# Kernel tuning notes

Measured on AMD Instinct MI355X. Metric: run time of the kernel, lower is better.

Reference implementation:

```python
import jax, jax.numpy as jnp
import numpy as np

VOCAB, D, SLOTS, K = 50257, 512, 16, 3
B, T_FULL = 64, 2049
EPS_LN = 1e-5


def setup_inputs() -> dict:
    key = jax.random.key(0)
    ks = jax.random.split(key, 12)
    u = jax.random.uniform(ks[0], (B, T_FULL - 1), jnp.float32)
    gumbel = -jnp.log(-jnp.log(u + 1e-8) + 1e-8)
    s = 0.02
    return {
        "seq": jax.random.randint(ks[1], (B, T_FULL), 0, VOCAB),
        "temperature": jnp.ones((), jnp.float32),
        "gumbel": gumbel,
        "embed": jax.random.normal(ks[2], (VOCAB, D), jnp.float32) * s,
        "W1": jax.random.normal(ks[3], (D, 2 * D), jnp.float32) * s,
        "b1": jnp.zeros((2 * D,), jnp.float32),
        "W2": jax.random.normal(ks[4], (2 * D, D), jnp.float32) * s,
        "b2": jnp.zeros((D,), jnp.float32),
        "gamma": jnp.ones((D,), jnp.float32),
        "beta": jnp.zeros((D,), jnp.float32),
        "Wg": jax.random.normal(ks[5], (D,), jnp.float32) * s,
        "bg": jnp.zeros((), jnp.float32),
        "Wr": jax.random.normal(ks[6], (D, D), jnp.float32) * s,
        "br": jnp.zeros((D,), jnp.float32),
        "Wo": jax.random.normal(ks[7], (D, VOCAB), jnp.float32) * s,
        "bo": jnp.zeros((VOCAB,), jnp.float32),
    }


def reference(seq, temperature, gumbel, embed, W1, b1, W2, b2, gamma, beta, Wg, bg, Wr, br, Wo, bo):
    # Encoder: embed -> FFN residual -> LayerNorm
    h = embed[seq]                                        # [B, T+1, D]
    ff = jnp.maximum(h @ W1 + b1, 0.0) @ W2 + b2
    x = h + ff
    mu = jnp.mean(x, -1, keepdims=True)
    var = jnp.mean((x - mu) ** 2, -1, keepdims=True)
    hiddens = (x - mu) * jax.lax.rsqrt(var + EPS_LN) * gamma + beta

    context = hiddens[:, :-1, :]                          # [B, T, D]
    gate = context @ Wg + bg                              # [B, T]

    # gumbel top-k with straight-through mask (forward value = hard mask)
    perturbed = (gate + gumbel) / temperature
    _, idx = jax.lax.top_k(perturbed, K)                  # [B, K]
    mask = jnp.zeros_like(gate).at[jnp.arange(B)[:, None], idx].set(1.0)
    soft = jax.nn.softmax(perturbed, axis=-1)
    sel = mask + soft - jax.lax.stop_gradient(soft)

    # gather selected hidden states, scatter_add into memory slots
    gw = jnp.take_along_axis(sel, idx, axis=1)            # [B, K]
    gh = jnp.take_along_axis(context, idx[..., None], axis=1)  # [B, K, D]
    weighted = gh * gw[..., None]
    slot_idx = jnp.arange(K) % SLOTS
    mem = jnp.zeros((B, SLOTS, D), hiddens.dtype).at[:, slot_idx, :].add(weighted)

    # attention read with last-position query
    q = hiddens[:, -1, :] @ Wr + br                       # [B, D]
    scores = jnp.einsum('bsd,bd->bs', mem, q)
    attn = jax.nn.softmax(scores, axis=-1)
    ctx = jnp.einsum('bs,bsd->bd', attn, mem)
    return ctx @ Wo + bo                                  # [B, vocab]
```

## Files before the change

kernel.cpp:

```cpp
#include <hip/hip_runtime.h>
#include <math.h>

#define TFULL 2049
#define TCTX  2048
#define Vm    50257

#define KBS 1032

typedef __attribute__((ext_vector_type(8))) short bf16x8;
typedef __attribute__((ext_vector_type(4))) short s16x4;
typedef __attribute__((ext_vector_type(4))) float f32x4;

__device__ __forceinline__ float wred64(float v){
  #pragma unroll
  for (int m = 1; m < 64; m <<= 1) v += __shfl_xor(v, m, 64);
  return v;
}
__device__ __forceinline__ short bf16_rn(float x){
  union { float f; unsigned u; } c; c.f = x;
  unsigned r = c.u + 0x7fff + ((c.u >> 16) & 1);
  return (short)(r >> 16);
}
__device__ __forceinline__ float bf16_f(short s){
  union { float f; unsigned u; } c; c.u = ((unsigned)(unsigned short)s) << 16;
  return c.f;
}

#define FMA4(ACC_, S_, W_)                         \
  (ACC_).x = fmaf((S_), (W_).x, (ACC_).x);         \
  (ACC_).y = fmaf((S_), (W_).y, (ACC_).y);         \
  (ACC_).z = fmaf((S_), (W_).z, (ACC_).z);         \
  (ACC_).w = fmaf((S_), (W_).w, (ACC_).w);

__global__ void k0_setup(const float* __restrict__ gamma, const float* __restrict__ beta,
                         const float* __restrict__ Wg, float* __restrict__ scal){
  const int t = threadIdx.x;
  float wg = Wg[t];
  float g  = gamma[t]*wg, bw = beta[t]*wg;
  scal[2 + t] = g;
  g = wred64(g); bw = wred64(bw);
  __shared__ float ra[8], rb[8];
  if ((t & 63) == 0){ ra[t>>6] = g; rb[t>>6] = bw; }
  __syncthreads();
  if (t == 0){
    float G = 0.f, Bw = 0.f;
    #pragma unroll
    for (int i = 0; i < 8; ++i){ G += ra[i]; Bw += rb[i]; }
    scal[0] = G; scal[1] = Bw;
  }
}

__global__ __launch_bounds__(256) void kpack(const float* __restrict__ W, int N, int KB,
                                             short* __restrict__ hi, short* __restrict__ lo){
  int i = blockIdx.x*256 + threadIdx.x;
  if (i >= KB*N*4) return;
  int kq = i & 3;
  int n  = (i >> 2) % N;
  int kb = i / (N*4);
  const float* src = W + (kb*32 + kq*8)*N + n;
  bf16x8 h8, l8;
  #pragma unroll
  for (int j = 0; j < 8; ++j){
    float w = src[j*N];
    short h = bf16_rn(w);
    h8[j] = h;
    l8[j] = bf16_rn(w - bf16_f(h));
  }
  *(bf16x8*)(hi + i*8) = h8;
  *(bf16x8*)(lo + i*8) = l8;
}

__global__ __launch_bounds__(512, 4) void k1_main(
    const int*   __restrict__ seq,   const float* __restrict__ temp,
    const float* __restrict__ gumbel,const float* __restrict__ embed,
    const short* __restrict__ W1h,   const short* __restrict__ W1l,
    const float* __restrict__ b1,
    const short* __restrict__ W2h,   const short* __restrict__ W2l,
    const float* __restrict__ b2,
    const float* __restrict__ gamma, const float* __restrict__ beta,
    const float* __restrict__ bg,
    const float* __restrict__ scal,
    float* __restrict__ pert, float* __restrict__ qh)
{
  __shared__ __align__(16) short Ah[8*KBS];
  __shared__ __align__(16) short Al[8*KBS];
  __shared__ __align__(16) short Rbuf[2*8*KBS];
  __shared__ float Xq[512];
  __shared__ int   srow[32];
  __shared__ float redS1[256], redS2[256], redSG[256];
  __shared__ float redMu[32], redRs[32];

  short* Rh = Rbuf;
  short* Rl = Rbuf + 8*KBS;

  const int t    = threadIdx.x;
  const int tile = blockIdx.x;
  const int lane = t & 63;
  const int wv   = t >> 6;
  const int mrow = lane & 15;
  const int kq   = lane >> 4;
  const int crow0 = kq*4;

  const int lane_sw = kq*128 + ((mrow & 12) | ((mrow ^ kq) & 3))*8;

  if (t < 32) srow[t] = seq[tile*32 + t];
  __syncthreads();

  const f32x4* __restrict__ embv = (const f32x4*)embed;

  auto stageA = [&](int hh){
    #pragma unroll
    for (int k = 0; k < 4; ++k){
      int idx = k*512 + t;
      int tok = idx >> 6, c4 = idx & 63;
      f32x4 v = embv[srow[tok]*128 + hh*64 + c4];
      int kbr = c4 >> 3, kqw = (c4 >> 1) & 3, j0 = (c4 & 1)*4;
      int tokL = tok & 15, mt = tok >> 4;
      int base = kbr*KBS + mt*512 + kqw*128
               + ((tokL & 12) | ((tokL ^ kqw) & 3))*8 + j0;
      short h0 = bf16_rn(v[0]), h1 = bf16_rn(v[1]), h2 = bf16_rn(v[2]), h3 = bf16_rn(v[3]);
      *(s16x4*)(Ah + base) = (s16x4){h0, h1, h2, h3};
      *(s16x4*)(Al + base) = (s16x4){ bf16_rn(v[0] - bf16_f(h0)),
                                      bf16_rn(v[1] - bf16_f(h1)),
                                      bf16_rn(v[2] - bf16_f(h2)),
                                      bf16_rn(v[3] - bf16_f(h3)) };
    }
  };

  f32x4 ff[4][2];
  #pragma unroll
  for (int i = 0; i < 4; ++i)
    #pragma unroll
    for (int j = 0; j < 2; ++j) ff[i][j] = (f32x4){0.f,0.f,0.f,0.f};

  int boff2[4];
  #pragma unroll
  for (int nt = 0; nt < 4; ++nt)
    boff2[nt] = (wv*64 + nt*16 + mrow)*32 + kq*8;

  #pragma unroll 1
  for (int ch = 0; ch < 4; ++ch){
    f32x4 acc[2][2];
    #pragma unroll
    for (int i = 0; i < 2; ++i)
      #pragma unroll
      for (int j = 0; j < 2; ++j) acc[i][j] = (f32x4){0.f,0.f,0.f,0.f};

    int boff1[2];
    #pragma unroll
    for (int nt = 0; nt < 2; ++nt)
      boff1[nt] = (ch*256 + wv*32 + nt*16 + mrow)*32 + kq*8;

    auto g1 = [&](int hh){
      const short* whB = W1h + hh*262144;
      const short* wlB = W1l + hh*262144;
      #pragma unroll
      for (int kbr = 0; kbr < 8; ++kbr){
        bf16x8 ah0 = *(const bf16x8*)(Ah + kbr*KBS + lane_sw);
        bf16x8 al0 = *(const bf16x8*)(Al + kbr*KBS + lane_sw);
        bf16x8 ah1 = *(const bf16x8*)(Ah + kbr*KBS + 512 + lane_sw);
        bf16x8 al1 = *(const bf16x8*)(Al + kbr*KBS + 512 + lane_sw);
        #pragma unroll
        for (int nt = 0; nt < 2; ++nt){
          bf16x8 bh = *(const bf16x8*)(whB + kbr*32768 + boff1[nt]);
          bf16x8 bl = *(const bf16x8*)(wlB + kbr*32768 + boff1[nt]);
          acc[nt][0] = __builtin_amdgcn_mfma_f32_16x16x32_bf16(ah0, bh, acc[nt][0], 0,0,0);
          acc[nt][0] = __builtin_amdgcn_mfma_f32_16x16x32_bf16(al0, bh, acc[nt][0], 0,0,0);
          acc[nt][0] = __builtin_amdgcn_mfma_f32_16x16x32_bf16(ah0, bl, acc[nt][0], 0,0,0);
          acc[nt][1] = __builtin_amdgcn_mfma_f32_16x16x32_bf16(ah1, bh, acc[nt][1], 0,0,0);
          acc[nt][1] = __builtin_amdgcn_mfma_f32_16x16x32_bf16(al1, bh, acc[nt][1], 0,0,0);
          acc[nt][1] = __builtin_amdgcn_mfma_f32_16x16x32_bf16(ah1, bl, acc[nt][1], 0,0,0);
        }
      }
    };

    stageA(0);
    __syncthreads();
    g1(0);
    __syncthreads();
    stageA(1);
    __syncthreads();
    g1(1);
    __syncthreads();

    #pragma unroll
    for (int nt = 0; nt < 2; ++nt){
      int jcol = wv*32 + nt*16 + mrow;
      float bb = b1[ch*256 + jcol];
      int kb2 = jcol >> 5, kq2 = (jcol >> 3) & 3, j2 = jcol & 7;
      int rbase = kb2*KBS + kq2*128 + j2;
      #pragma unroll
      for (int mt = 0; mt < 2; ++mt){
        #pragma unroll
        for (int r = 0; r < 4; ++r){
          int tokL = crow0 + r;
          int off = rbase + mt*512 + ((tokL & 12) | ((tokL ^ kq2) & 3))*8;
          float a = fmaxf(acc[nt][mt][r] + bb, 0.f);
          short h = bf16_rn(a);
          Rh[off] = h;
          Rl[off] = bf16_rn(a - bf16_f(h));
        }
      }
    }
    __syncthreads();

    {
      const short* w2hB = W2h + ch*131072;
      const short* w2lB = W2l + ch*131072;
      #pragma unroll
      for (int kb = 0; kb < 8; ++kb){
        bf16x8 rh0 = *(const bf16x8*)(Rh + kb*KBS + lane_sw);
        bf16x8 rl0 = *(const bf16x8*)(Rl + kb*KBS + lane_sw);
        bf16x8 rh1 = *(const bf16x8*)(Rh + kb*KBS + 512 + lane_sw);
        bf16x8 rl1 = *(const bf16x8*)(Rl + kb*KBS + 512 + lane_sw);
        #pragma unroll
        for (int nt = 0; nt < 4; ++nt){
          bf16x8 bh = *(const bf16x8*)(w2hB + kb*16384 + boff2[nt]);
          bf16x8 bl = *(const bf16x8*)(w2lB + kb*16384 + boff2[nt]);
          ff[nt][0] = __builtin_amdgcn_mfma_f32_16x16x32_bf16(rh0, bh, ff[nt][0], 0,0,0);
          ff[nt][0] = __builtin_amdgcn_mfma_f32_16x16x32_bf16(rl0, bh, ff[nt][0], 0,0,0);
          ff[nt][0] = __builtin_amdgcn_mfma_f32_16x16x32_bf16(rh0, bl, ff[nt][0], 0,0,0);
          ff[nt][1] = __builtin_amdgcn_mfma_f32_16x16x32_bf16(rh1, bh, ff[nt][1], 0,0,0);
          ff[nt][1] = __builtin_amdgcn_mfma_f32_16x16x32_bf16(rl1, bh, ff[nt][1], 0,0,0);
          ff[nt][1] = __builtin_amdgcn_mfma_f32_16x16x32_bf16(rh1, bl, ff[nt][1], 0,0,0);
        }
      }
    }
  }

  __syncthreads();
  float* hbuf = (float*)Rbuf;
  #pragma unroll
  for (int k = 0; k < 4; ++k){
    int idx = k*512 + t;
    int tok = idx >> 6, c4 = idx & 63;
    f32x4 v = embv[srow[tok]*128 + c4];
    f32x4 hv;
    #pragma unroll
    for (int j = 0; j < 4; ++j){
      short hi = bf16_rn(v[j]);
      hv[j] = bf16_f(hi) + bf16_f(bf16_rn(v[j] - bf16_f(hi)));
    }
    *(f32x4*)(hbuf + tok*256 + c4*4) = hv;
  }
  __syncthreads();

  const float G1 = scal[0], BW = scal[1];
  const float* gWg = scal + 2;
  const float bgv  = bg[0];
  const float invT = 1.0f / temp[0];
  int rem  = (tile*32) % 2049;
  int qtok = 2048 - rem;

  float ps1[2][4], ps2[2][4], psg[2][4];
  #pragma unroll
  for (int mt = 0; mt < 2; ++mt)
    #pragma unroll
    for (int r = 0; r < 4; ++r){ ps1[mt][r]=0.f; ps2[mt][r]=0.f; psg[mt][r]=0.f; }

  #pragma unroll
  for (int nt = 0; nt < 4; ++nt){
    int d = wv*64 + nt*16 + mrow;
    float b2v = b2[d];
    float gw  = gWg[d];
    if (wv >= 4){
      int dl = d - 256;
      int kbr = dl >> 5, kq2 = (dl >> 3) & 3, jj = dl & 7;
      int abase = kbr*KBS + kq2*128 + jj;
      #pragma unroll
      for (int mt = 0; mt < 2; ++mt){
        #pragma unroll
        for (int r = 0; r < 4; ++r){
          int tokL = crow0 + r;
          int tok  = mt*16 + tokL;
          int off  = abase + mt*512 + ((tokL & 12) | ((tokL ^ kq2) & 3))*8;
          float h = bf16_f(Ah[off]) + bf16_f(Al[off]);
          float x = h + ff[nt][mt][r] + b2v;
          ps1[mt][r] += x;
          ps2[mt][r] = fmaf(x, x, ps2[mt][r]);
          psg[mt][r] = fmaf(x, gw, psg[mt][r]);
          if (tok == qtok) Xq[d] = x;
        }
      }
    } else {
      #pragma unroll
      for (int mt = 0; mt < 2; ++mt){
        #pragma unroll
        for (int r = 0; r < 4; ++r){
          int tok = mt*16 + crow0 + r;
          float h = hbuf[tok*256 + d];
          float x = h + ff[nt][mt][r] + b2v;
          ps1[mt][r] += x;
          ps2[mt][r] = fmaf(x, x, ps2[mt][r]);
          psg[mt][r] = fmaf(x, gw, psg[mt][r]);
          if (tok == qtok) Xq[d] = x;
        }
      }
    }
  }
  #pragma unroll
  for (int mt = 0; mt < 2; ++mt){
    #pragma unroll
    for (int r = 0; r < 4; ++r){
      float a = ps1[mt][r], b = ps2[mt][r], c = psg[mt][r];
      #pragma unroll
      for (int m = 1; m < 16; m <<= 1){
        a += __shfl_xor(a, m, 64);
        b += __shfl_xor(b, m, 64);
        c += __shfl_xor(c, m, 64);
      }
      if (mrow == 0){
        int tok = mt*16 + crow0 + r;
        redS1[tok*8 + wv] = a;
        redS2[tok*8 + wv] = b;
        redSG[tok*8 + wv] = c;
      }
    }
  }
  __syncthreads();

  if (t < 32){
    float S1 = 0.f, S2 = 0.f, SG = 0.f;
    #pragma unroll
    for (int w = 0; w < 8; ++w){
      S1 += redS1[t*8 + w];
      S2 += redS2[t*8 + w];
      SG += redSG[t*8 + w];
    }
    float mu  = S1 * (1.f/512.f);
    float var = S2 * (1.f/512.f) - mu*mu;
    float rs  = rsqrtf(var + 1e-5f);
    redMu[t] = mu; redRs[t] = rs;
    int id  = tile*32 + t;
    int b   = id / 2049;
    int pos = id - b*2049;
    if (pos < TCTX){
      float gate = rs*(SG - mu*G1) + BW + bgv;
      float pv = (gate + __builtin_nontemporal_load(gumbel + b*TCTX + pos)) * invT;
      __builtin_nontemporal_store(pv, pert + b*TCTX + pos);
    }
  }
  __syncthreads();

  if (qtok < 32 && t < 256){
    int id = tile*32 + qtok;
    int b  = id / 2049;
    float mu = redMu[qtok], rs = redRs[qtok];
    int d = t*2;
    qh[b*512 + d]     = (Xq[d]  -mu)*rs*gamma[d]   + beta[d];
    qh[b*512 + d + 1] = (Xq[d+1]-mu)*rs*gamma[d+1] + beta[d+1];
  }
}

__global__ __launch_bounds__(256) void k2_topk(const float* __restrict__ pert,
                                               int* __restrict__ idxw){
  __shared__ float v[2048];
  __shared__ float wvv[256];
  __shared__ int   wii[256];
  const int b = blockIdx.x, t = threadIdx.x;
  for (int i = t; i < 2048; i += 256) v[i] = pert[b*TCTX + i];
  __syncthreads();
  for (int r = 0; r < 3; ++r){
    float best = -INFINITY; int bi = 1<<30;
    for (int i = t; i < 2048; i += 256){
      float x = v[i];
      if (x > best || (x == best && i < bi)){ best = x; bi = i; }
    }
    wvv[t] = best; wii[t] = bi;
    __syncthreads();
    for (int s = 128; s > 0; s >>= 1){
      if (t < s){
        float ov = wvv[t+s]; int oi = wii[t+s];
        if (ov > wvv[t] || (ov == wvv[t] && oi < wii[t])){ wvv[t] = ov; wii[t] = oi; }
      }
      __syncthreads();
    }
    if (t == 0){ idxw[b*3 + r] = wii[0]; v[wii[0]] = -INFINITY; }
    __syncthreads();
  }
}

__global__ __launch_bounds__(256) void k3_rows(const int* __restrict__ seq,
    const float* __restrict__ embed, const float* __restrict__ W1, const float* __restrict__ b1,
    const float* __restrict__ W2,    const float* __restrict__ b2,
    const float* __restrict__ gamma, const float* __restrict__ beta,
    const int* __restrict__ idxw, float* __restrict__ memr)
{
  __shared__ float hs[3*512];
  __shared__ float rbuf[3*1024];
  __shared__ float red1[12], red2[12];
  const int t  = threadIdx.x;
  const int b  = blockIdx.x;
  const int wv = t >> 6;
  #pragma unroll
  for (int kk = 0; kk < 3; ++kk){
    int pos = idxw[b*3 + kk];
    int row = seq[b*TFULL + pos];
    ((float2*)(hs + kk*512))[t] = ((const float2*)(embed + row*512))[t];
  }
  __syncthreads();
  const float4* W1v = (const float4*)W1;
  float4 a0 = make_float4(0,0,0,0), a1 = a0, a2 = a0;
  #pragma unroll 2
  for (int d = 0; d < 512; ++d){
    float4 wq = W1v[d*256 + t];
    float h0 = hs[d], h1 = hs[512+d], h2 = hs[1024+d];
    FMA4(a0, h0, wq); FMA4(a1, h1, wq); FMA4(a2, h2, wq);
  }
  float4 bq = ((const float4*)b1)[t];
  float4 r0, r1, r2;
  r0.x = fmaxf(a0.x+bq.x,0.f); r0.y = fmaxf(a0.y+bq.y,0.f);
  r0.z = fmaxf(a0.z+bq.z,0.f); r0.w = fmaxf(a0.w+bq.w,0.f);
  r1.x = fmaxf(a1.x+bq.x,0.f); r1.y = fmaxf(a1.y+bq.y,0.f);
  r1.z = fmaxf(a1.z+bq.z,0.f); r1.w = fmaxf(a1.w+bq.w,0.f);
  r2.x = fmaxf(a2.x+bq.x,0.f); r2.y = fmaxf(a2.y+bq.y,0.f);
  r2.z = fmaxf(a2.z+bq.z,0.f); r2.w = fmaxf(a2.w+bq.w,0.f);
  ((float4*)rbuf)[t]          = r0;
  ((float4*)(rbuf+1024))[t]   = r1;
  ((float4*)(rbuf+2048))[t]   = r2;
  __syncthreads();
  const float2* W2v2 = (const float2*)W2;
  float f0x=0.f,f0y=0.f,f1x=0.f,f1y=0.f,f2x=0.f,f2y=0.f;
  #pragma unroll 2
  for (int j = 0; j < 1024; ++j){
    float2 wq = W2v2[j*256 + t];
    float q0 = rbuf[j], q1 = rbuf[1024+j], q2 = rbuf[2048+j];
    f0x = fmaf(q0, wq.x, f0x); f0y = fmaf(q0, wq.y, f0y);
    f1x = fmaf(q1, wq.x, f1x); f1y = fmaf(q1, wq.y, f1y);
    f2x = fmaf(q2, wq.x, f2x); f2y = fmaf(q2, wq.y, f2y);
  }
  float2 b2q = ((const float2*)b2)[t];
  const int dd = t*2;
  float2 hx0 = ((float2*)hs)[t];
  float2 hx1 = ((float2*)(hs+512))[t];
  float2 hx2 = ((float2*)(hs+1024))[t];
  float x00 = hx0.x + f0x + b2q.x, x01 = hx0.y + f0y + b2q.y;
  float x10 = hx1.x + f1x + b2q.x, x11 = hx1.y + f1y + b2q.y;
  float x20 = hx2.x + f2x + b2q.x, x21 = hx2.y + f2y + b2q.y;
  float s10 = wred64(x00 + x01), s20 = wred64(x00*x00 + x01*x01);
  float s11 = wred64(x10 + x11), s21 = wred64(x10*x10 + x11*x11);
  float s12 = wred64(x20 + x21), s22 = wred64(x20*x20 + x21*x21);
  if ((t & 63) == 0){
    red1[0*4+wv] = s10; red2[0*4+wv] = s20;
    red1[1*4+wv] = s11; red2[1*4+wv] = s21;
    red1[2*4+wv] = s12; red2[2*4+wv] = s22;
  }
  __syncthreads();
  float gx = gamma[dd], gy = gamma[dd+1], bx = beta[dd], by = beta[dd+1];
  #pragma unroll
  for (int kk = 0; kk < 3; ++kk){
    float S1 = red1[kk*4+0]+red1[kk*4+1]+red1[kk*4+2]+red1[kk*4+3];
    float S2 = red2[kk*4+0]+red2[kk*4+1]+red2[kk*4+2]+red2[kk*4+3];
    float mu  = S1*(1.f/512.f);
    float var = S2*(1.f/512.f) - mu*mu;
    float rs  = rsqrtf(var + 1e-5f);
    float x0 = (kk==0) ? x00 : (kk==1) ? x10 : x20;
    float x1 = (kk==0) ? x01 : (kk==1) ? x11 : x21;
    memr[(b*3+kk)*512 + dd]     = (x0-mu)*rs*gx + bx;
    memr[(b*3+kk)*512 + dd + 1] = (x1-mu)*rs*gy + by;
  }
}

__global__ __launch_bounds__(256) void k4_attn(const float* __restrict__ qh,
    const float* __restrict__ Wr, const float* __restrict__ br,
    const float* __restrict__ memr, float* __restrict__ ctxT)
{
  __shared__ float hq[512];
  __shared__ float red[12];
  const int t = threadIdx.x, b = blockIdx.x;
  ((float2*)hq)[t] = ((const float2*)(qh + b*512))[t];
  __syncthreads();
  const float2* Wrv = (const float2*)Wr;
  float qx = 0.f, qy = 0.f;
  #pragma unroll 4
  for (int d = 0; d < 512; ++d){
    float hb = hq[d];
    float2 wq = Wrv[d*256 + t];
    qx = fmaf(hb, wq.x, qx); qy = fmaf(hb, wq.y, qy);
  }
  float2 brq = ((const float2*)br)[t];
  qx += brq.x; qy += brq.y;
  const int dd = t*2;
  const float* m0 = memr + (b*3+0)*512;
  const float* m1 = memr + (b*3+1)*512;
  const float* m2 = memr + (b*3+2)*512;
  float p0 = wred64(qx*m0[dd] + qy*m0[dd+1]);
  float p1 = wred64(qx*m1[dd] + qy*m1[dd+1]);
  float p2 = wred64(qx*m2[dd] + qy*m2[dd+1]);
  if ((t & 63) == 0){ int w = t>>6; red[w*3+0]=p0; red[w*3+1]=p1; red[w*3+2]=p2; }
  __syncthreads();
  float s0 = red[0]+red[3]+red[6]+red[9];
  float s1 = red[1]+red[4]+red[7]+red[10];
  float s2 = red[2]+red[5]+red[8]+red[11];
  float m  = fmaxf(fmaxf(s0, s1), fmaxf(s2, 0.f));
  float e0 = expf(s0-m), e1 = expf(s1-m), e2 = expf(s2-m);
  float den = e0 + e1 + e2 + 13.f*expf(-m);
  float a0 = e0/den, a1 = e1/den, a2 = e2/den;
  float c0 = a0*m0[dd]   + a1*m1[dd]   + a2*m2[dd];
  float c1 = a0*m0[dd+1] + a1*m1[dd+1] + a2*m2[dd+1];
  ctxT[dd*64 + b]     = c0;
  ctxT[(dd+1)*64 + b] = c1;
}

__global__ __launch_bounds__(256) void k5_out(const float* __restrict__ ctxT,
    const float* __restrict__ Wo, const float* __restrict__ bo,
    float* __restrict__ out)
{
  const int v  = blockIdx.x*256 + threadIdx.x;
  const int vc = v < Vm ? v : Vm-1;
  float acc[64];
  #pragma unroll
  for (int b = 0; b < 64; ++b) acc[b] = 0.f;
  for (int d = 0; d < 512; ++d){
    float w = Wo[d*Vm + vc];
    const float* c = ctxT + d*64;
    #pragma unroll
    for (int b = 0; b < 64; ++b) acc[b] = fmaf(c[b], w, acc[b]);
  }
  if (v < Vm){
    float bb = bo[v];
    #pragma unroll
    for (int b = 0; b < 64; ++b) out[b*Vm + v] = acc[b] + bb;
  }
}

extern "C" void kernel_launch(void* const* d_in, const int* in_sizes, int n_in,
                              void* d_out, int out_size, void* d_ws, size_t ws_size,
                              hipStream_t stream){
  (void)in_sizes; (void)n_in; (void)out_size; (void)ws_size;
  const int*   seq   = (const int*)d_in[0];
  const float* temp  = (const float*)d_in[1];
  const float* gum   = (const float*)d_in[2];
  const float* embed = (const float*)d_in[3];
  const float* W1    = (const float*)d_in[4];
  const float* b1    = (const float*)d_in[5];
  const float* W2    = (const float*)d_in[6];
  const float* b2    = (const float*)d_in[7];
  const float* gamma = (const float*)d_in[8];
  const float* beta  = (const float*)d_in[9];
  const float* Wg    = (const float*)d_in[10];
  const float* bg    = (const float*)d_in[11];
  const float* Wr    = (const float*)d_in[12];
  const float* br    = (const float*)d_in[13];
  const float* Wo    = (const float*)d_in[14];
  const float* bo    = (const float*)d_in[15];
  float* out = (float*)d_out;

  float* wsf  = (float*)d_ws;
  float* pert = wsf;
  float* qh   = wsf + 131072;
  float* memr = wsf + 163840;
  float* ctxT = wsf + 262144;
  float* scal = wsf + 294912;
  int*   idxw = (int*)(wsf + 295936);
  short* W1h  = (short*)(wsf + 296192);
  short* W1l  = W1h + 512*1024;
  short* W2h  = W1l + 512*1024;
  short* W2l  = W2h + 1024*512;

  k0_setup<<<1, 512, 0, stream>>>(gamma, beta, Wg, scal);
  kpack<<<256, 256, 0, stream>>>(W1, 1024, 16, W1h, W1l);
  kpack<<<256, 256, 0, stream>>>(W2, 512, 32, W2h, W2l);
  k1_main<<<4098, 512, 0, stream>>>(seq, temp, gum, embed, W1h, W1l, b1,
                                    W2h, W2l, b2, gamma, beta, bg, scal, pert, qh);
  k2_topk<<<64, 256, 0, stream>>>(pert, idxw);
  k3_rows<<<64, 256, 0, stream>>>(seq, embed, W1, b1, W2, b2, gamma, beta, idxw, memr);
  k4_attn<<<64, 256, 0, stream>>>(qh, Wr, br, memr, ctxT);
  k5_out<<<197, 256, 0, stream>>>(ctxT, Wo, bo, out);
}
```

Baseline: 2.071 ms.

## Stage full embedding tile once in LDS and reuse across all chunks

```diff
diff --git a/kernel.cpp b/kernel.cpp
--- a/kernel.cpp
+++ b/kernel.cpp
@@ -70,7 +70,7 @@
   *(bf16x8*)(lo + i*8) = l8;
 }
 
-__global__ __launch_bounds__(512, 4) void k1_main(
+__global__ __launch_bounds__(512, 2) void k1_main(
     const int*   __restrict__ seq,   const float* __restrict__ temp,
     const float* __restrict__ gumbel,const float* __restrict__ embed,
     const short* __restrict__ W1h,   const short* __restrict__ W1l,
@@ -82,8 +82,8 @@
     const float* __restrict__ scal,
     float* __restrict__ pert, float* __restrict__ qh)
 {
-  __shared__ __align__(16) short Ah[8*KBS];
-  __shared__ __align__(16) short Al[8*KBS];
+  __shared__ __align__(16) short Ah[16*KBS];
+  __shared__ __align__(16) short Al[16*KBS];
   __shared__ __align__(16) short Rbuf[2*8*KBS];
   __shared__ float Xq[512];
   __shared__ int   srow[32];
@@ -108,24 +108,23 @@
 
   const f32x4* __restrict__ embv = (const f32x4*)embed;
 
-  auto stageA = [&](int hh){
-    #pragma unroll
-    for (int k = 0; k < 4; ++k){
-      int idx = k*512 + t;
-      int tok = idx >> 6, c4 = idx & 63;
-      f32x4 v = embv[srow[tok]*128 + hh*64 + c4];
-      int kbr = c4 >> 3, kqw = (c4 >> 1) & 3, j0 = (c4 & 1)*4;
-      int tokL = tok & 15, mt = tok >> 4;
-      int base = kbr*KBS + mt*512 + kqw*128
-               + ((tokL & 12) | ((tokL ^ kqw) & 3))*8 + j0;
-      short h0 = bf16_rn(v[0]), h1 = bf16_rn(v[1]), h2 = bf16_rn(v[2]), h3 = bf16_rn(v[3]);
-      *(s16x4*)(Ah + base) = (s16x4){h0, h1, h2, h3};
-      *(s16x4*)(Al + base) = (s16x4){ bf16_rn(v[0] - bf16_f(h0)),
-                                      bf16_rn(v[1] - bf16_f(h1)),
-                                      bf16_rn(v[2] - bf16_f(h2)),
-                                      bf16_rn(v[3] - bf16_f(h3)) };
-    }
-  };
+  #pragma unroll
+  for (int k = 0; k < 8; ++k){
+    int idx = k*512 + t;
+    int tok = idx >> 7, c4 = idx & 127;
+    f32x4 v = embv[srow[tok]*128 + c4];
+    int kbr = c4 >> 3, kqw = (c4 >> 1) & 3, j0 = (c4 & 1)*4;
+    int tokL = tok & 15, mt = tok >> 4;
+    int base = kbr*KBS + mt*512 + kqw*128
+             + ((tokL & 12) | ((tokL ^ kqw) & 3))*8 + j0;
+    short h0 = bf16_rn(v[0]), h1 = bf16_rn(v[1]), h2 = bf16_rn(v[2]), h3 = bf16_rn(v[3]);
+    *(s16x4*)(Ah + base) = (s16x4){h0, h1, h2, h3};
+    *(s16x4*)(Al + base) = (s16x4){ bf16_rn(v[0] - bf16_f(h0)),
+                                    bf16_rn(v[1] - bf16_f(h1)),
+                                    bf16_rn(v[2] - bf16_f(h2)),
+                                    bf16_rn(v[3] - bf16_f(h3)) };
+  }
+  __syncthreads();
 
   f32x4 ff[4][2];
   #pragma unroll
@@ -151,36 +150,25 @@
     for (int nt = 0; nt < 2; ++nt)
       boff1[nt] = (ch*256 + wv*32 + nt*16 + mrow)*32 + kq*8;
 
-    auto g1 = [&](int hh){
-      const short* whB = W1h + hh*262144;
-      const short* wlB = W1l + hh*262144;
+    #pragma unroll 4
+    for (int kbr = 0; kbr < 16; ++kbr){
+      bf16x8 ah0 = *(const bf16x8*)(Ah + kbr*KBS + lane_sw);
+      bf16x8 al0 = *(const bf16x8*)(Al + kbr*KBS + lane_sw);
+      bf16x8 ah1 = *(const bf16x8*)(Ah + kbr*KBS + 512 + lane_sw);
+      bf16x8 al1 = *(const bf16x8*)(Al + kbr*KBS + 512 + lane_sw);
       #pragma unroll
-      for (int kbr = 0; kbr < 8; ++kbr){
-        bf16x8 ah0 = *(const bf16x8*)(Ah + kbr*KBS + lane_sw);
-        bf16x8 al0 = *(const bf16x8*)(Al + kbr*KBS + lane_sw);
-        bf16x8 ah1 = *(const bf16x8*)(Ah + kbr*KBS + 512 + lane_sw);
-        bf16x8 al1 = *(const bf16x8*)(Al + kbr*KBS + 512 + lane_sw);
-        #pragma unroll
-        for (int nt = 0; nt < 2; ++nt){
-          bf16x8 bh = *(const bf16x8*)(whB + kbr*32768 + boff1[nt]);
-          bf16x8 bl = *(const bf16x8*)(wlB + kbr*32768 + boff1[nt]);
-          acc[nt][0] = __builtin_amdgcn_mfma_f32_16x16x32_bf16(ah0, bh, acc[nt][0], 0,0,0);
-          acc[nt][0] = __builtin_amdgcn_mfma_f32_16x16x32_bf16(al0, bh, acc[nt][0], 0,0,0);
-          acc[nt][0] = __builtin_amdgcn_mfma_f32_16x16x32_bf16(ah0, bl, acc[nt][0], 0,0,0);
-          acc[nt][1] = __builtin_amdgcn_mfma_f32_16x16x32_bf16(ah1, bh, acc[nt][1], 0,0,0);
-          acc[nt][1] = __builtin_amdgcn_mfma_f32_16x16x32_bf16(al1, bh, acc[nt][1], 0,0,0);
-          acc[nt][1] = __builtin_amdgcn_mfma_f32_16x16x32_bf16(ah1, bl, acc[nt][1], 0,0,0);
-        }
-      }
-    };
-
-    stageA(0);
-    __syncthreads();
-    g1(0);
-    __syncthreads();
-    stageA(1);
-    __syncthreads();
-    g1(1);
+      for (int nt = 0; nt < 2; ++nt){
+        bf16x8 bh = *(const bf16x8*)(W1h + kbr*32768 + boff1[nt]);
+        bf16x8 bl = *(const bf16x8*)(W1l + kbr*32768 + boff1[nt]);
+        acc[nt][0] = __builtin_amdgcn_mfma_f32_16x16x32_bf16(ah0, bh, acc[nt][0], 0,0,0);
+        acc[nt][0] = __builtin_amdgcn_mfma_f32_16x16x32_bf16(al0, bh, acc[nt][0], 0,0,0);
+        acc[nt][0] = __builtin_amdgcn_mfma_f32_16x16x32_bf16(ah0, bl, acc[nt][0], 0,0,0);
+        acc[nt][1] = __builtin_amdgcn_mfma_f32_16x16x32_bf16(ah1, bh, acc[nt][1], 0,0,0);
+        acc[nt][1] = __builtin_amdgcn_mfma_f32_16x16x32_bf16(al1, bh, acc[nt][1], 0,0,0);
+        acc[nt][1] = __builtin_amdgcn_mfma_f32_16x16x32_bf16(ah1, bl, acc[nt][1], 0,0,0);
+      }
+    }
+
     __syncthreads();
 
     #pragma unroll
@@ -207,7 +195,7 @@
     {
       const short* w2hB = W2h + ch*131072;
       const short* w2lB = W2l + ch*131072;
-      #pragma unroll
+      #pragma unroll 2
       for (int kb = 0; kb < 8; ++kb){
         bf16x8 rh0 = *(const bf16x8*)(Rh + kb*KBS + lane_sw);
         bf16x8 rl0 = *(const bf16x8*)(Rl + kb*KBS + lane_sw);
@@ -228,23 +216,6 @@
     }
   }
 
-  __syncthreads();
-  float* hbuf = (float*)Rbuf;
-  #pragma unroll
-  for (int k = 0; k < 4; ++k){
-    int idx = k*512 + t;
-    int tok = idx >> 6, c4 = idx & 63;
-    f32x4 v = embv[srow[tok]*128 + c4];
-    f32x4 hv;
-    #pragma unroll
-    for (int j = 0; j < 4; ++j){
-      short hi = bf16_rn(v[j]);
-      hv[j] = bf16_f(hi) + bf16_f(bf16_rn(v[j] - bf16_f(hi)));
-    }
-    *(f32x4*)(hbuf + tok*256 + c4*4) = hv;
-  }
-  __syncthreads();
-
   const float G1 = scal[0], BW = scal[1];
   const float* gWg = scal + 2;
   const float bgv  = bg[0];
@@ -263,38 +234,21 @@
     int d = wv*64 + nt*16 + mrow;
     float b2v = b2[d];
     float gw  = gWg[d];
-    if (wv >= 4){
-      int dl = d - 256;
-      int kbr = dl >> 5, kq2 = (dl >> 3) & 3, jj = dl & 7;
-      int abase = kbr*KBS + kq2*128 + jj;
+    int kb  = d >> 5, kq2 = (d >> 3) & 3, jj = d & 7;
+    int abase = kb*KBS + kq2*128 + jj;
+    #pragma unroll
+    for (int mt = 0; mt < 2; ++mt){
       #pragma unroll
-      for (int mt = 0; mt < 2; ++mt){
-        #pragma unroll
-        for (int r = 0; r < 4; ++r){
-          int tokL = crow0 + r;
-          int tok  = mt*16 + tokL;
-          int off  = abase + mt*512 + ((tokL & 12) | ((tokL ^ kq2) & 3))*8;
-          float h = bf16_f(Ah[off]) + bf16_f(Al[off]);
-          float x = h + ff[nt][mt][r] + b2v;
-          ps1[mt][r] += x;
-          ps2[mt][r] = fmaf(x, x, ps2[mt][r]);
-          psg[mt][r] = fmaf(x, gw, psg[mt][r]);
-          if (tok == qtok) Xq[d] = x;
-        }
-      }
-    } else {
-      #pragma unroll
-      for (int mt = 0; mt < 2; ++mt){
-        #pragma unroll
-        for (int r = 0; r < 4; ++r){
-          int tok = mt*16 + crow0 + r;
-          float h = hbuf[tok*256 + d];
-          float x = h + ff[nt][mt][r] + b2v;
-          ps1[mt][r] += x;
-          ps2[mt][r] = fmaf(x, x, ps2[mt][r]);
-          psg[mt][r] = fmaf(x, gw, psg[mt][r]);
-          if (tok == qtok) Xq[d] = x;
-        }
+      for (int r = 0; r < 4; ++r){
+        int tokL = crow0 + r;
+        int tok  = mt*16 + tokL;
+        int off  = abase + mt*512 + ((tokL & 12) | ((tokL ^ kq2) & 3))*8;
+        float h = bf16_f(Ah[off]) + bf16_f(Al[off]);
+        float x = h + ff[nt][mt][r] + b2v;
+        ps1[mt][r] += x;
+        ps2[mt][r] = fmaf(x, x, ps2[mt][r]);
+        psg[mt][r] = fmaf(x, gw, psg[mt][r]);
+        if (tok == qtok) Xq[d] = x;
       }
     }
   }
```

After: 2.473 ms. +19.5%, slower.
